# Kernel optimization log

Measured on AMD Instinct MI355X. Metric: run time of the kernel, lower is better.

Reference implementation:

```python
import jax, jax.numpy as jnp
import numpy as np

HIDDEN = 1024
N_HEADS = 16
HEAD_DIM = HIDDEN // N_HEADS


def setup_inputs() -> dict:
    key = jax.random.key(0)
    ks = jax.random.split(key, 7)
    b, l, m = 4, 1024, 1024
    q = jax.random.normal(ks[0], (b, l, HIDDEN), dtype=jnp.float32)
    k = jax.random.normal(ks[1], (b, m, HIDDEN), dtype=jnp.float32)
    v = jax.random.normal(ks[2], (b, m, HIDDEN), dtype=jnp.float32)
    s = 1.0 / np.sqrt(HIDDEN)
    w_q = jax.random.normal(ks[3], (HIDDEN, HIDDEN), dtype=jnp.float32) * s
    w_k = jax.random.normal(ks[4], (HIDDEN, HIDDEN), dtype=jnp.float32) * s
    w_v = jax.random.normal(ks[5], (HIDDEN, HIDDEN), dtype=jnp.float32) * s
    w_o = jax.random.normal(ks[6], (HIDDEN, HIDDEN), dtype=jnp.float32) * s
    return {"q": q, "k": k, "v": v, "w_q": w_q, "w_k": w_k, "w_v": w_v, "w_o": w_o}


def reference(q, k, v, w_q, w_k, w_v, w_o):
    b, l, _ = q.shape
    _, m, _ = k.shape
    # Linear (bias=False): y = x @ W^T
    qp = q @ w_q.T
    kp = k @ w_k.T
    vp = v @ w_v.T  # projected but unused downstream (faithful to original bug)
    # Faithful non-standard split: hidden -> (head_dim, n_heads)
    qh = qp.reshape(b, l, HEAD_DIM, N_HEADS)
    kh = kp.reshape(b, m, HEAD_DIM, N_HEADS)
    # attn over K, scaled, softmax over m (dim=2)
    scores = jnp.einsum('bldn,bmdn->blmn', qh, kh) / np.sqrt(HEAD_DIM)
    attn = jax.nn.softmax(scores, axis=2)
    # dropout is identity in eval mode
    # NOTE: original attends over K (not V) — reproduced faithfully
    x = jnp.einsum('blmn,bmdn->bldn', attn, kh)
    x = x.reshape(b, l, HIDDEN)  # 'b l d n -> b l (d n)'
    return x @ w_o.T
```

## Files before the change

### kernel.cpp

```cpp
#include <hip/hip_runtime.h>
#include <hip/hip_bf16.h>
#include <stdint.h>
#include <math.h>


typedef __bf16 bf16;
typedef __bf16 bf16x8 __attribute__((ext_vector_type(8)));
typedef __bf16 bf16x4 __attribute__((ext_vector_type(4)));
typedef float  f32x4  __attribute__((ext_vector_type(4)));
typedef float  f32x16 __attribute__((ext_vector_type(16)));

__device__ __forceinline__ void async_load16(const void* g, void* l) {
  __builtin_amdgcn_global_load_lds((__attribute__((address_space(1))) void*)g,
                                   (__attribute__((address_space(3))) void*)l,
                                   16, 0, 0);
}

__device__ __forceinline__ void join_pin() {
  __builtin_amdgcn_sched_barrier(0);
  __builtin_amdgcn_s_barrier();
  __builtin_amdgcn_sched_barrier(0);
}

__device__ __forceinline__ int detect_fl(const void* samp, int tid, int* smax) {
  int e = (((const unsigned short*)samp)[tid] >> 7) & 0xFF;
#pragma unroll
  for (int off = 1; off <= 32; off <<= 1) {
    int o = __shfl_xor(e, off);
    e = o > e ? o : e;
  }
  if ((tid & 63) == 0) smax[tid >> 6] = e;
  __syncthreads();
  int m01 = smax[0] > smax[1] ? smax[0] : smax[1];
  int m23 = smax[2] > smax[3] ? smax[2] : smax[3];
  return ((m01 > m23 ? m01 : m23) >= 140) ? 1 : 0;
}

__global__ void __launch_bounds__(256)
canon(const void* __restrict__ q, const void* __restrict__ k,
      const void* __restrict__ wq, const void* __restrict__ wk,
      const void* __restrict__ wo,
      bf16* __restrict__ qc, bf16* __restrict__ kc,
      bf16* __restrict__ wqc, bf16* __restrict__ wkc,
      bf16* __restrict__ wo_p, int* __restrict__ flag) {
  __shared__ int smax[4];
  const int tid = threadIdx.x;
  const int fl = detect_fl(q, tid, smax);
  if (blockIdx.x == 0 && tid == 0) *flag = fl;

  const size_t e0 = (size_t)blockIdx.x * 2048 + tid * 8;
  const size_t M4 = 4194304, M8 = 8388608, M9 = 9437184, M10 = 10485760;
  const void* src; bf16* dst; size_t le; bool perm = false;
  if (e0 < M4)       { src = q;  dst = qc;   le = e0;       }
  else if (e0 < M8)  { src = k;  dst = kc;   le = e0 - M4;  }
  else if (e0 < M9)  { src = wq; dst = wqc;  le = e0 - M8;  }
  else if (e0 < M10) { src = wk; dst = wkc;  le = e0 - M9;  }
  else               { src = wo; dst = wo_p; le = e0 - M10; perm = true; }

  if (!perm) {
    bf16x8 v;
    if (fl) {
      const float* p = (const float*)src + le;
      f32x4 a = *(const f32x4*)p, b = *(const f32x4*)(p + 4);
#pragma unroll
      for (int j = 0; j < 4; ++j) { v[j] = (bf16)a[j]; v[4 + j] = (bf16)b[j]; }
    } else {
      v = *(const bf16x8*)((const bf16*)src + le);
    }
    *(bf16x8*)(dst + le) = v;
  } else {
    int o = (int)(le >> 10), kp0 = (int)(le & 1023);
    bf16x8 v;
#pragma unroll
    for (int j = 0; j < 8; ++j) {
      int kp = kp0 + j;
      int h = ((kp & 63) << 4) | (kp >> 6);
      float f = fl ? ((const float*)src)[o * 1024 + h]
                   : (float)((const bf16*)src)[o * 1024 + h];
      f = fminf(fmaxf(f, -1024.f), 1024.f);
      v[j] = (bf16)f;
    }
    *(bf16x8*)(dst + le) = v;
  }
}

__global__ void __launch_bounds__(256, 2)
qk_gemm(const bf16* __restrict__ qc, const bf16* __restrict__ wqc,
        const bf16* __restrict__ kc, const bf16* __restrict__ wkc,
        bf16* __restrict__ qh, bf16* __restrict__ kh, bf16* __restrict__ khT,
        float cs) {
  __shared__ __align__(16) char smem[65536];
  bf16* const sA0 = (bf16*)smem;
  bf16* const sA1 = (bf16*)(smem + 16384);
  bf16* const sB0 = (bf16*)(smem + 32768);
  bf16* const sB1 = (bf16*)(smem + 49152);
  bf16* const epi = (bf16*)smem;

  const int tid  = threadIdx.x;
  const int lane = tid & 63;
  const int wave = tid >> 6;
  const int q4   = lane >> 4;
  const int c16  = lane & 15;
  const int wm   = wave >> 1;
  const int wn   = wave & 1;

  const int z = blockIdx.z;
  const bf16* A = z ? kc : qc;
  const bf16* W = z ? wkc : wqc;
  const float scale = z ? 1.0f : cs;
  bf16* out0 = z ? kh : qh;

  const int lin    = blockIdx.x + 8 * blockIdx.y;
  const int rowBlk = (lin & 31) * 128;
  const int colBlk = (lin >> 5) * 128;

  const bf16* gA[4]; const bf16* gB[4]; int lS[4];
#pragma unroll
  for (int i = 0; i < 4; ++i) {
    int s = tid + 256 * i;
    int r = s >> 3, g = (s & 7) ^ (r & 7);
    gA[i] = A + (size_t)(rowBlk + r) * 1024 + g * 8;
    gB[i] = W + (size_t)(colBlk + r) * 1024 + g * 8;
    lS[i] = s * 8;
  }

  f32x4 acc[4][4] = {};

#pragma unroll
  for (int i = 0; i < 4; ++i) async_load16(gA[i], sA0 + lS[i]);
#pragma unroll
  for (int i = 0; i < 4; ++i) async_load16(gB[i], sB0 + lS[i]);

  for (int t = 0; t < 16; ++t) {
    if (t < 15) {
      const int kn = (t + 1) * 64;
      bf16* dA = (t & 1) ? sA0 : sA1;
      bf16* dB = (t & 1) ? sB0 : sB1;
#pragma unroll
      for (int i = 0; i < 4; ++i) async_load16(gA[i] + kn, dA + lS[i]);
#pragma unroll
      for (int i = 0; i < 4; ++i) async_load16(gB[i] + kn, dB + lS[i]);
      asm volatile("s_waitcnt vmcnt(8)" ::: "memory");
    } else {
      asm volatile("s_waitcnt vmcnt(0)" ::: "memory");
    }
    join_pin();

    const bf16* cA = (t & 1) ? sA1 : sA0;
    const bf16* cB = (t & 1) ? sB1 : sB0;
#pragma unroll
    for (int ks = 0; ks < 2; ++ks) {
      bf16x8 af[4], bfr[4];
#pragma unroll
      for (int mt = 0; mt < 4; ++mt) {
        int row = wm * 64 + mt * 16 + c16;
        af[mt] = *(const bf16x8*)(cA + row * 64 +
                   (((ks * 4 + q4) ^ (row & 7)) * 8));
      }
#pragma unroll
      for (int nt = 0; nt < 4; ++nt) {
        int row = wn * 64 + nt * 16 + c16;
        bfr[nt] = *(const bf16x8*)(cB + row * 64 +
                   (((ks * 4 + q4) ^ (row & 7)) * 8));
      }
#pragma unroll
      for (int mt = 0; mt < 4; ++mt)
#pragma unroll
        for (int nt = 0; nt < 4; ++nt)
          acc[mt][nt] = __builtin_amdgcn_mfma_f32_16x16x32_bf16(
              af[mt], bfr[nt], acc[mt][nt], 0, 0, 0);
    }
    asm volatile("s_waitcnt lgkmcnt(0)" ::: "memory");
    join_pin();
  }

#pragma unroll
  for (int mt = 0; mt < 4; ++mt)
#pragma unroll
    for (int nt = 0; nt < 4; ++nt)
#pragma unroll
      for (int r = 0; r < 4; ++r) {
        int m_t = wm * 64 + mt * 16 + q4 * 4 + r;
        int h_t = wn * 64 + nt * 16 + c16;
        epi[m_t * 134 + h_t] = (bf16)(acc[mt][nt][r] * scale);
      }
  __syncthreads();

  const int bb    = rowBlk >> 10;
  const int mbase = rowBlk & 1023;
  const int dg0   = colBlk >> 4;

  {
    int n = tid >> 4;
#pragma unroll
    for (int i = 0; i < 8; ++i) {
      int m_t = (tid & 15) + i * 16;
      bf16x8 v;
#pragma unroll
      for (int dt = 0; dt < 8; ++dt) v[dt] = epi[m_t * 134 + dt * 16 + n];
      *(bf16x8*)(out0 + ((size_t)(bb * 16 + n) * 1024 + mbase + m_t) * 64 + dg0) = v;
    }
  }
  if (z) {
    int h_t = tid >> 1, half = tid & 1;
    int n = h_t & 15, dt = h_t >> 4;
    size_t base = ((size_t)(bb * 16 + n) * 64 + dg0 + dt) * 1024 + mbase + half * 64;
#pragma unroll
    for (int c = 0; c < 8; ++c) {
      bf16x8 v;
#pragma unroll
      for (int j = 0; j < 8; ++j) v[j] = epi[(half * 64 + c * 8 + j) * 134 + h_t];
      *(bf16x8*)(khT + base + c * 8) = v;
    }
  }
}

__global__ void __launch_bounds__(256, 2)
attn_kernel(const bf16* __restrict__ qh, const bf16* __restrict__ kh,
            const bf16* __restrict__ khT, bf16* __restrict__ xh) {
  __shared__ __align__(16) bf16 sK[2][64 * 64];
  __shared__ __align__(16) bf16 sKT[2][64 * 64];
  __shared__ __align__(16) bf16 sP[4][32 * 72];

  const int tid  = threadIdx.x;
  const int lane = tid & 63;
  const int wave = tid >> 6;
  const int n32  = lane & 31;
  const int hk   = lane >> 5;
  const int lin  = blockIdx.x;
  const int bn   = lin & 63;
  const int qt   = lin >> 6;
  const int b    = bn >> 4, n = bn & 15;
  const int l0w  = qt * 128 + wave * 32;

  const bf16* qhead  = qh  + (size_t)bn * (1024 * 64);
  const bf16* khead  = kh  + (size_t)bn * (1024 * 64);
  const bf16* kThead = khT + (size_t)bn * (64 * 1024);

  bf16x8 aq[4];
#pragma unroll
  for (int kc = 0; kc < 4; ++kc)
    aq[kc] = *(const bf16x8*)(qhead + (size_t)(l0w + n32) * 64 + kc * 16 + hk * 8);

  int kr[2], kg[2];
#pragma unroll
  for (int i = 0; i < 2; ++i) {
    int s = tid + 256 * i;
    kr[i] = s >> 3;  kg[i] = (s & 7) ^ (kr[i] & 7);
  }

  f32x16 O[2] = {};
  f32x16 Osum = {};
  bf16x8 ones;
#pragma unroll
  for (int j = 0; j < 8; ++j) ones[j] = (bf16)1.0f;
  bf16* sPw = sP[wave];

#pragma unroll
  for (int i = 0; i < 2; ++i) {
    int s = (tid + 256 * i) * 8;
    async_load16(khead + (size_t)kr[i] * 64 + kg[i] * 8, &sK[0][s]);
    async_load16(kThead + (size_t)kr[i] * 1024 + kg[i] * 8, &sKT[0][s]);
  }

  for (int t = 0; t < 16; ++t) {
    if (t < 15) {
      const int m0n = (t + 1) * 64;
      const int bi  = (t + 1) & 1;
#pragma unroll
      for (int i = 0; i < 2; ++i) {
        int s = (tid + 256 * i) * 8;
        async_load16(khead + (size_t)(m0n + kr[i]) * 64 + kg[i] * 8, &sK[bi][s]);
        async_load16(kThead + (size_t)kr[i] * 1024 + m0n + kg[i] * 8, &sKT[bi][s]);
      }
      asm volatile("s_waitcnt vmcnt(4)" ::: "memory");
    } else {
      asm volatile("s_waitcnt vmcnt(0)" ::: "memory");
    }
    join_pin();

    const bf16* cK  = sK[t & 1];
    const bf16* cKT = sKT[t & 1];

    f32x16 S0 = {}, S1 = {};
    __builtin_amdgcn_s_setprio(1);
#pragma unroll
    for (int kc = 0; kc < 4; ++kc) {
      int G = kc * 2 + hk;
      int R0 = n32, R1 = 32 + n32;
      bf16x8 bk0 = *(const bf16x8*)(cK + R0 * 64 + ((G ^ (R0 & 7)) * 8));
      bf16x8 bk1 = *(const bf16x8*)(cK + R1 * 64 + ((G ^ (R1 & 7)) * 8));
      S0 = __builtin_amdgcn_mfma_f32_32x32x16_bf16(aq[kc], bk0, S0, 0, 0, 0);
      S1 = __builtin_amdgcn_mfma_f32_32x32x16_bf16(aq[kc], bk1, S1, 0, 0, 0);
    }
    __builtin_amdgcn_s_setprio(0);

#pragma unroll
    for (int r = 0; r < 16; ++r) {
      int qrow = (r & 3) + 8 * (r >> 2) + 4 * hk;
      sPw[qrow * 72 + n32]      = (bf16)__builtin_amdgcn_exp2f(S0[r]);
      sPw[qrow * 72 + 32 + n32] = (bf16)__builtin_amdgcn_exp2f(S1[r]);
    }

    bf16x8 ap[4];
    __builtin_amdgcn_s_setprio(1);
#pragma unroll
    for (int kc = 0; kc < 4; ++kc) {
      ap[kc] = *(const bf16x8*)(sPw + n32 * 72 + kc * 16 + hk * 8);
      Osum = __builtin_amdgcn_mfma_f32_32x32x16_bf16(ap[kc], ones, Osum, 0, 0, 0);
    }
#pragma unroll
    for (int dt = 0; dt < 2; ++dt) {
#pragma unroll
      for (int kc = 0; kc < 4; ++kc) {
        int R = dt * 32 + n32;
        int G = kc * 2 + hk;
        bf16x8 bkt = *(const bf16x8*)(cKT + R * 64 + ((G ^ (R & 7)) * 8));
        O[dt] = __builtin_amdgcn_mfma_f32_32x32x16_bf16(ap[kc], bkt, O[dt], 0, 0, 0);
      }
    }
    __builtin_amdgcn_s_setprio(0);
    asm volatile("s_waitcnt lgkmcnt(0)" ::: "memory");
    join_pin();
  }

  {
    float inv[16];
#pragma unroll
    for (int r = 0; r < 16; ++r) inv[r] = 1.0f / Osum[r];
#pragma unroll
    for (int dt = 0; dt < 2; ++dt)
#pragma unroll
      for (int r = 0; r < 16; ++r) {
        int qrow = (r & 3) + 8 * (r >> 2) + 4 * hk;
        sPw[qrow * 72 + dt * 32 + n32] = (bf16)(O[dt][r] * inv[r]);
      }
  }
  {
    int l_loc = lane >> 1, dh = lane & 1;
    size_t base = ((size_t)(b * 1024 + l0w + l_loc) * 16 + n) * 64 + dh * 32;
#pragma unroll
    for (int c8 = 0; c8 < 4; ++c8) {
      bf16x8 v = *(const bf16x8*)(sPw + l_loc * 72 + dh * 32 + c8 * 8);
      *(bf16x8*)(xh + base + c8 * 8) = v;
    }
  }
}

__global__ void __launch_bounds__(256, 4)
o_gemm(const bf16* __restrict__ A, const bf16* __restrict__ W,
       bf16* __restrict__ out0, float* __restrict__ outf,
       const int* __restrict__ flag) {
  __shared__ __align__(16) bf16 sA[2][64 * 64];
  __shared__ __align__(16) bf16 sB[2][64 * 64];

  const int tid  = threadIdx.x;
  const int lane = tid & 63;
  const int wave = tid >> 6;
  const int q4   = lane >> 4;
  const int c16  = lane & 15;
  const int wm   = wave >> 1;
  const int wn   = wave & 1;

  const int lin    = blockIdx.x + 8 * blockIdx.y;
  const int rowBlk = (lin & 63) * 64;
  const int colBlk = (lin >> 6) * 64;

  const bf16* gA[2]; const bf16* gB[2]; int ls[2];
#pragma unroll
  for (int i = 0; i < 2; ++i) {
    int s = tid + 256 * i;
    int r = s >> 3, g = (s & 7) ^ (r & 7);
    gA[i] = A + (size_t)(rowBlk + r) * 1024 + g * 8;
    gB[i] = W + (size_t)(colBlk + r) * 1024 + g * 8;
    ls[i] = s * 8;
  }

  f32x4 acc[2][2] = {};

#pragma unroll
  for (int i = 0; i < 2; ++i) {
    async_load16(gA[i], &sA[0][ls[i]]);
    async_load16(gB[i], &sB[0][ls[i]]);
  }

  for (int t = 0; t < 16; ++t) {
    if (t < 15) {
      const int kn = (t + 1) * 64;
      const int bi = (t + 1) & 1;
#pragma unroll
      for (int i = 0; i < 2; ++i) {
        async_load16(gA[i] + kn, &sA[bi][ls[i]]);
        async_load16(gB[i] + kn, &sB[bi][ls[i]]);
      }
      asm volatile("s_waitcnt vmcnt(4)" ::: "memory");
    } else {
      asm volatile("s_waitcnt vmcnt(0)" ::: "memory");
    }
    join_pin();

    const bf16* cA = sA[t & 1];
    const bf16* cB = sB[t & 1];
#pragma unroll
    for (int ks = 0; ks < 2; ++ks) {
      bf16x8 af[2], bfr[2];
#pragma unroll
      for (int mt = 0; mt < 2; ++mt) {
        int row = wm * 32 + mt * 16 + c16;
        af[mt] = *(const bf16x8*)(cA + row * 64 +
                   (((ks * 4 + q4) ^ (row & 7)) * 8));
      }
#pragma unroll
      for (int nt = 0; nt < 2; ++nt) {
        int row = wn * 32 + nt * 16 + c16;
        bfr[nt] = *(const bf16x8*)(cB + row * 64 +
                   (((ks * 4 + q4) ^ (row & 7)) * 8));
      }
#pragma unroll
      for (int mt = 0; mt < 2; ++mt)
#pragma unroll
        for (int nt = 0; nt < 2; ++nt)
          acc[mt][nt] = __builtin_amdgcn_mfma_f32_16x16x32_bf16(
              af[mt], bfr[nt], acc[mt][nt], 0, 0, 0);
    }
    asm volatile("s_waitcnt lgkmcnt(0)" ::: "memory");
    join_pin();
  }

  const int fl = *flag;
#pragma unroll
  for (int mt = 0; mt < 2; ++mt)
#pragma unroll
    for (int nt = 0; nt < 2; ++nt)
#pragma unroll
      for (int r = 0; r < 4; ++r) {
        int gm = rowBlk + wm * 32 + mt * 16 + q4 * 4 + r;
        int gn = colBlk + wn * 32 + nt * 16 + c16;
        size_t idx = (size_t)gm * 1024 + gn;
        if (fl) outf[idx] = acc[mt][nt][r];
        else    out0[idx] = (bf16)acc[mt][nt][r];
      }
}

extern "C" void kernel_launch(void* const* d_in, const int* in_sizes, int n_in,
                              void* d_out, int out_size, void* d_ws, size_t ws_size,
                              hipStream_t stream) {
  const void* q_raw  = d_in[0];
  const void* k_raw  = d_in[1];
  const void* wq_raw = d_in[3];
  const void* wk_raw = d_in[4];
  const void* wo_raw = d_in[6];

  char* ws = (char*)d_ws;
  const size_t MB = 1024 * 1024;
  bf16* qc   = (bf16*)(ws + 0 * MB);
  bf16* kc   = (bf16*)(ws + 8 * MB);
  bf16* kh   = (bf16*)(ws + 16 * MB);
  bf16* wqc  = (bf16*)(ws + 24 * MB);
  bf16* wkc  = (bf16*)(ws + 26 * MB);
  bf16* wo_p = (bf16*)(ws + 28 * MB);
  int*  flag = (int*)(ws + 30 * MB);
  bf16* xh   = qc;
  bf16* qh   = (bf16*)d_out;
  bf16* khT  = (bf16*)((char*)d_out + 8 * MB);

  const float CS = 0.125f * 1.4426950408889634f;
  dim3 blk(256, 1, 1);

  hipLaunchKernelGGL(canon, dim3(5632), blk, 0, stream,
                     q_raw, k_raw, wq_raw, wk_raw, wo_raw,
                     qc, kc, wqc, wkc, wo_p, flag);
  hipLaunchKernelGGL(qk_gemm, dim3(8, 32, 2), blk, 0, stream,
                     qc, wqc, kc, wkc, qh, kh, khT, CS);
  hipLaunchKernelGGL(attn_kernel, dim3(512), blk, 0, stream,
                     qh, kh, khT, xh);
  hipLaunchKernelGGL(o_gemm, dim3(8, 128), blk, 0, stream,
                     xh, wo_p, (bf16*)d_out, (float*)d_out, flag);
}
```

Baseline: 182.6 us.

## Triple-buffer attention K tiles and enlarge output GEMM row tile

The attention kernel moves from a double-buffered K/K^T pipeline to a three-stage ring that prefetches two tiles ahead. This leaves one barrier per iteration instead of two, removing sync stalls and hiding more load latency at the cost of more LDS per block. Separately, the output projection GEMM now uses a 128x64 tile per block with launch bounds lowered to 3 and half as many blocks. That raises A-operand reuse per B load, but reduces block count and occupancy.

```diff
diff --git a/kernel.cpp b/kernel.cpp
--- a/kernel.cpp
+++ b/kernel.cpp
@@ -218,8 +218,8 @@
 __global__ void __launch_bounds__(256, 2)
 attn_kernel(const bf16* __restrict__ qh, const bf16* __restrict__ kh,
             const bf16* __restrict__ khT, bf16* __restrict__ xh) {
-  __shared__ __align__(16) bf16 sK[2][64 * 64];
-  __shared__ __align__(16) bf16 sKT[2][64 * 64];
+  __shared__ __align__(16) bf16 sK[3][64 * 64];
+  __shared__ __align__(16) bf16 sKT[3][64 * 64];
   __shared__ __align__(16) bf16 sP[4][32 * 72];
 
   const int tid  = threadIdx.x;
@@ -256,31 +256,34 @@
   for (int j = 0; j < 8; ++j) ones[j] = (bf16)1.0f;
   bf16* sPw = sP[wave];
 
-#pragma unroll
-  for (int i = 0; i < 2; ++i) {
-    int s = (tid + 256 * i) * 8;
-    async_load16(khead + (size_t)kr[i] * 64 + kg[i] * 8, &sK[0][s]);
-    async_load16(kThead + (size_t)kr[i] * 1024 + kg[i] * 8, &sKT[0][s]);
-  }
-
+  auto stage = [&](int tt, int bi) {
+    const int m0 = tt * 64;
+#pragma unroll
+    for (int i = 0; i < 2; ++i) {
+      int s = (tid + 256 * i) * 8;
+      async_load16(khead + (size_t)(m0 + kr[i]) * 64 + kg[i] * 8, &sK[bi][s]);
+      async_load16(kThead + (size_t)kr[i] * 1024 + m0 + kg[i] * 8, &sKT[bi][s]);
+    }
+  };
+
+  stage(0, 0);
+  stage(1, 1);
+
+  int cur = 0;
   for (int t = 0; t < 16; ++t) {
-    if (t < 15) {
-      const int m0n = (t + 1) * 64;
-      const int bi  = (t + 1) & 1;
-#pragma unroll
-      for (int i = 0; i < 2; ++i) {
-        int s = (tid + 256 * i) * 8;
-        async_load16(khead + (size_t)(m0n + kr[i]) * 64 + kg[i] * 8, &sK[bi][s]);
-        async_load16(kThead + (size_t)kr[i] * 1024 + m0n + kg[i] * 8, &sKT[bi][s]);
-      }
-      asm volatile("s_waitcnt vmcnt(4)" ::: "memory");
-    } else {
-      asm volatile("s_waitcnt vmcnt(0)" ::: "memory");
-    }
+    if (t < 15) asm volatile("s_waitcnt vmcnt(4)" ::: "memory");
+    else        asm volatile("s_waitcnt vmcnt(0)" ::: "memory");
+    asm volatile("s_waitcnt lgkmcnt(0)" ::: "memory");
     join_pin();
 
-    const bf16* cK  = sK[t & 1];
-    const bf16* cKT = sKT[t & 1];
+    if (t < 14) {
+      int nx = cur + 2;
+      if (nx >= 3) nx -= 3;
+      stage(t + 2, nx);
+    }
+
+    const bf16* cK  = sK[cur];
+    const bf16* cKT = sKT[cur];
 
     f32x16 S0 = {}, S1 = {};
     __builtin_amdgcn_s_setprio(1);
@@ -320,8 +323,8 @@
       }
     }
     __builtin_amdgcn_s_setprio(0);
-    asm volatile("s_waitcnt lgkmcnt(0)" ::: "memory");
-    join_pin();
+
+    cur = (cur == 2) ? 0 : cur + 1;
   }
 
   {
@@ -347,12 +350,15 @@
   }
 }
 
-__global__ void __launch_bounds__(256, 4)
+__global__ void __launch_bounds__(256, 3)
 o_gemm(const bf16* __restrict__ A, const bf16* __restrict__ W,
        bf16* __restrict__ out0, float* __restrict__ outf,
        const int* __restrict__ flag) {
-  __shared__ __align__(16) bf16 sA[2][64 * 64];
-  __shared__ __align__(16) bf16 sB[2][64 * 64];
+  __shared__ __align__(16) char smem[49152];
+  bf16* const sA0 = (bf16*)smem;
+  bf16* const sA1 = (bf16*)(smem + 16384);
+  bf16* const sB0 = (bf16*)(smem + 32768);
+  bf16* const sB1 = (bf16*)(smem + 40960);
 
   const int tid  = threadIdx.x;
   const int lane = tid & 63;
@@ -363,50 +369,56 @@
   const int wn   = wave & 1;
 
   const int lin    = blockIdx.x + 8 * blockIdx.y;
-  const int rowBlk = (lin & 63) * 64;
-  const int colBlk = (lin >> 6) * 64;
-
-  const bf16* gA[2]; const bf16* gB[2]; int ls[2];
+  const int rowBlk = (lin & 31) * 128;
+  const int colBlk = (lin >> 5) * 64;
+
+  const bf16* gA[4]; int lA[4];
+#pragma unroll
+  for (int i = 0; i < 4; ++i) {
+    int s = tid + 256 * i;
+    int r = s >> 3, g = (s & 7) ^ (r & 7);
+    gA[i] = A + (size_t)(rowBlk + r) * 1024 + g * 8;
+    lA[i] = s * 8;
+  }
+  const bf16* gB[2]; int lB[2];
 #pragma unroll
   for (int i = 0; i < 2; ++i) {
     int s = tid + 256 * i;
     int r = s >> 3, g = (s & 7) ^ (r & 7);
-    gA[i] = A + (size_t)(rowBlk + r) * 1024 + g * 8;
     gB[i] = W + (size_t)(colBlk + r) * 1024 + g * 8;
-    ls[i] = s * 8;
-  }
-
-  f32x4 acc[2][2] = {};
-
-#pragma unroll
-  for (int i = 0; i < 2; ++i) {
-    async_load16(gA[i], &sA[0][ls[i]]);
-    async_load16(gB[i], &sB[0][ls[i]]);
-  }
+    lB[i] = s * 8;
+  }
+
+  f32x4 acc[4][2] = {};
+
+#pragma unroll
+  for (int i = 0; i < 4; ++i) async_load16(gA[i], sA0 + lA[i]);
+#pragma unroll
+  for (int i = 0; i < 2; ++i) async_load16(gB[i], sB0 + lB[i]);
 
   for (int t = 0; t < 16; ++t) {
     if (t < 15) {
       const int kn = (t + 1) * 64;
-      const int bi = (t + 1) & 1;
-#pragma unroll
-      for (int i = 0; i < 2; ++i) {
-        async_load16(gA[i] + kn, &sA[bi][ls[i]]);
-        async_load16(gB[i] + kn, &sB[bi][ls[i]]);
-      }
-      asm volatile("s_waitcnt vmcnt(4)" ::: "memory");
+      bf16* dA = (t & 1) ? sA0 : sA1;
+      bf16* dB = (t & 1) ? sB0 : sB1;
+#pragma unroll
+      for (int i = 0; i < 4; ++i) async_load16(gA[i] + kn, dA + lA[i]);
+#pragma unroll
+      for (int i = 0; i < 2; ++i) async_load16(gB[i] + kn, dB + lB[i]);
+      asm volatile("s_waitcnt vmcnt(6)" ::: "memory");
     } else {
       asm volatile("s_waitcnt vmcnt(0)" ::: "memory");
     }
     join_pin();
 
-    const bf16* cA = sA[t & 1];
-    const bf16* cB = sB[t & 1];
+    const bf16* cA = (t & 1) ? sA1 : sA0;
+    const bf16* cB = (t & 1) ? sB1 : sB0;
 #pragma unroll
     for (int ks = 0; ks < 2; ++ks) {
-      bf16x8 af[2], bfr[2];
-#pragma unroll
-      for (int mt = 0; mt < 2; ++mt) {
-        int row = wm * 32 + mt * 16 + c16;
+      bf16x8 af[4], bfr[2];
+#pragma unroll
+      for (int mt = 0; mt < 4; ++mt) {
+        int row = wm * 64 + mt * 16 + c16;
         af[mt] = *(const bf16x8*)(cA + row * 64 +
                    (((ks * 4 + q4) ^ (row & 7)) * 8));
       }
@@ -417,7 +429,7 @@
                    (((ks * 4 + q4) ^ (row & 7)) * 8));
       }
 #pragma unroll
-      for (int mt = 0; mt < 2; ++mt)
+      for (int mt = 0; mt < 4; ++mt)
 #pragma unroll
         for (int nt = 0; nt < 2; ++nt)
           acc[mt][nt] = __builtin_amdgcn_mfma_f32_16x16x32_bf16(
@@ -429,12 +441,12 @@
 
   const int fl = *flag;
 #pragma unroll
-  for (int mt = 0; mt < 2; ++mt)
+  for (int mt = 0; mt < 4; ++mt)
 #pragma unroll
     for (int nt = 0; nt < 2; ++nt)
 #pragma unroll
       for (int r = 0; r < 4; ++r) {
-        int gm = rowBlk + wm * 32 + mt * 16 + q4 * 4 + r;
+        int gm = rowBlk + wm * 64 + mt * 16 + q4 * 4 + r;
         int gn = colBlk + wn * 32 + nt * 16 + c16;
         size_t idx = (size_t)gm * 1024 + gn;
         if (fl) outf[idx] = acc[mt][nt][r];
@@ -474,6 +486,6 @@
                      qc, wqc, kc, wkc, qh, kh, khT, CS);
   hipLaunchKernelGGL(attn_kernel, dim3(512), blk, 0, stream,
                      qh, kh, khT, xh);
-  hipLaunchKernelGGL(o_gemm, dim3(8, 128), blk, 0, stream,
+  hipLaunchKernelGGL(o_gemm, dim3(8, 64), blk, 0, stream,
                      xh, wo_p, (bf16*)d_out, (float*)d_out, flag);
 }
```

After: 174.7 us. 1.05x faster.
